# Performance work log

Measured on AMD Instinct MI355X. Metric: run time of the kernel, lower is better.

The kernel has to match this reference:

```python
import jax, jax.numpy as jnp
import numpy as np

A, S, D, V = 128, 512, 768, 30522
NL, LW = 10, 5  # n label categories, words per category
MASK_ID = 103
NEG = -1e30


def setup_inputs() -> dict:
    key = jax.random.key(0)
    ks = jax.random.split(key, 12)
    scale = 0.02
    input_ids = jax.random.randint(ks[0], (A, S), 0, 30000)
    input_ids = jnp.where(input_ids == MASK_ID, MASK_ID + 1, input_ids)  # strip accidental masks
    mask_pos = jax.random.randint(ks[1], (A,), 1, 3)  # one [MASK] per row, before position 3
    input_ids = input_ids.at[jnp.arange(A), mask_pos].set(MASK_ID)
    length = jax.random.randint(ks[2], (A,), 1, 400)
    bert_out = jax.random.normal(ks[3], (A, S, D), jnp.float32)
    label_words = jax.random.randint(ks[4], (NL, LW), 0, V)
    return {
        "bert_out": bert_out,
        "input_ids": input_ids,
        "length": length,
        "label_words": label_words,
        "W_senti": jax.random.normal(ks[5], (2, D), jnp.float32) * scale,
        "b_senti": jnp.zeros((2,), jnp.float32),
        "W_dense": jax.random.normal(ks[6], (D, 2 * D), jnp.float32) * scale,
        "b_dense": jnp.zeros((D,), jnp.float32),
        "W_prob": jax.random.normal(ks[7], (V, D), jnp.float32) * scale,
        "b_prob": jnp.zeros((V,), jnp.float32),
        "W_lab": jax.random.normal(ks[8], (NL, 2, LW), jnp.float32) * scale,
    }


def reference(bert_out, input_ids, length, label_words,
              W_senti, b_senti, W_dense, b_dense, W_prob, b_prob, W_lab):
    a, s, d = bert_out.shape
    # pooler = [CLS] hidden state -> senti head (dropout is identity in eval)
    senti_out = bert_out[:, 0] @ W_senti.T + b_senti  # [A,2]

    # gather the (single) [MASK] token hidden state per sample
    mask_pos = jnp.argmax(input_ids == MASK_ID, axis=1)        # [A]
    mask_logit = bert_out[jnp.arange(a), mask_pos]             # [A,D]

    # ragged attention pool over bert_out[i, 3:3+length[i]] vectorized via masking
    pos = jnp.arange(s)
    valid = (pos[None, :] >= 3) & (pos[None, :] < 3 + length[:, None])  # [A,S]
    scores = jnp.einsum('asd,ad->as', bert_out, mask_logit)
    scores = jnp.where(valid, scores, NEG)
    w = jax.nn.softmax(scores, axis=1)                         # [A,S]
    att = jnp.einsum('as,asd->ad', w, bert_out)                # [A,D]

    x = jnp.concatenate([att, mask_logit], axis=-1)            # [A,2D]
    h = jnp.tanh(x @ W_dense.T + b_dense)                      # [A,D]
    p = jnp.tanh(h @ W_prob.T + b_prob)                        # [A,V]

    # per-category label-word gather + small no-bias linear, stacked on dim 2
    lp = p[:, label_words]                                     # [A,NL,LW]
    out = jnp.einsum('alw,lkw->akl', lp, W_lab)                # [A,2,NL]
    return senti_out, out
```

## Files before the change

kernel.cpp:

```cpp
#include <hip/hip_runtime.h>
#include <stdint.h>

#define A_ 128
#define S_ 512
#define D_ 768
#define MASKID 103

typedef short bf16x8_t __attribute__((ext_vector_type(8)));
typedef float floatx4_t __attribute__((ext_vector_type(4)));

__device__ __forceinline__ unsigned short f2bf(float f) {
    union { unsigned int u; float f; } v; v.f = f;
    unsigned int u = v.u;
    return (unsigned short)((u + 0x7fffu + ((u >> 16) & 1u)) >> 16);
}

__global__ __launch_bounds__(256) void attn_part(
    const float* __restrict__ bert,
    const int* __restrict__ ids,
    const int* __restrict__ length,
    const int* __restrict__ label_words,
    const float* __restrict__ W_prob,
    const float* __restrict__ b_prob,
    unsigned short* __restrict__ ws_Wpw,
    float* __restrict__ ws_bp,
    int* __restrict__ ws_mask_pos,
    float* __restrict__ part_m,
    float* __restrict__ part_l,
    float* __restrict__ part_acc)
{
    int bx = blockIdx.x;
    int tid = threadIdx.x;
    if (bx >= A_ * 8) {
        int r = bx - A_ * 8;
        if (r < 50) {
            int word = label_words[r];
            const float* src = W_prob + (size_t)word * D_;
            for (int j = tid; j < D_; j += 256) ws_Wpw[r * D_ + j] = f2bf(src[j]);
            if (tid == 0) ws_bp[r] = b_prob[word];
        } else {
            for (int j = tid; j < D_; j += 256) ws_Wpw[r * D_ + j] = 0;
            if (tid == 0) ws_bp[r] = 0.f;
        }
        return;
    }
    int a = bx >> 3, c = bx & 7;
    int wave = tid >> 6, lane = tid & 63;
    int d0 = lane * 4;

    __shared__ int s_minpos;
    __shared__ float red_m[4], red_l[4];
    __shared__ float red_acc[4][D_];

    if (tid == 0) s_minpos = S_;
    __syncthreads();
    for (int p = tid; p < S_; p += 256)
        if (ids[a * S_ + p] == MASKID) atomicMin(&s_minpos, p);
    __syncthreads();
    int mp = (s_minpos >= S_) ? 0 : s_minpos;

    const float* base = bert + (size_t)a * S_ * D_;

    float ml[12];
    {
        const float* q = base + (size_t)mp * D_ + d0;
        float4 v0 = *(const float4*)(q);
        float4 v1 = *(const float4*)(q + 256);
        float4 v2 = *(const float4*)(q + 512);
        ml[0]=v0.x; ml[1]=v0.y; ml[2]=v0.z; ml[3]=v0.w;
        ml[4]=v1.x; ml[5]=v1.y; ml[6]=v1.z; ml[7]=v1.w;
        ml[8]=v2.x; ml[9]=v2.y; ml[10]=v2.z; ml[11]=v2.w;
    }
    int len = length[a]; if (len > S_ - 3) len = S_ - 3;

    float m = -3.0e38f, l = 0.f;
    float acc[12];
#pragma unroll
    for (int k = 0; k < 12; k++) acc[k] = 0.f;

    int v = c + 8 * wave;
    for (; v + 32 < len; v += 64) {
        const float* qa = base + (size_t)(3 + v) * D_ + d0;
        const float* qb = base + (size_t)(3 + v + 32) * D_ + d0;
        float4 a0 = *(const float4*)(qa);
        float4 a1 = *(const float4*)(qa + 256);
        float4 a2 = *(const float4*)(qa + 512);
        float4 b0 = *(const float4*)(qb);
        float4 b1 = *(const float4*)(qb + 256);
        float4 b2 = *(const float4*)(qb + 512);
        float ra[12], rb[12];
        ra[0]=a0.x; ra[1]=a0.y; ra[2]=a0.z; ra[3]=a0.w;
        ra[4]=a1.x; ra[5]=a1.y; ra[6]=a1.z; ra[7]=a1.w;
        ra[8]=a2.x; ra[9]=a2.y; ra[10]=a2.z; ra[11]=a2.w;
        rb[0]=b0.x; rb[1]=b0.y; rb[2]=b0.z; rb[3]=b0.w;
        rb[4]=b1.x; rb[5]=b1.y; rb[6]=b1.z; rb[7]=b1.w;
        rb[8]=b2.x; rb[9]=b2.y; rb[10]=b2.z; rb[11]=b2.w;
        float pa = 0.f, pb = 0.f;
#pragma unroll
        for (int k = 0; k < 12; k++) { pa = fmaf(ra[k], ml[k], pa); pb = fmaf(rb[k], ml[k], pb); }
#pragma unroll
        for (int off = 32; off >= 1; off >>= 1) {
            pa += __shfl_xor(pa, off, 64);
            pb += __shfl_xor(pb, off, 64);
        }
        float mn = fmaxf(m, fmaxf(pa, pb));
        float alpha = __expf(m - mn);
        float wa = __expf(pa - mn);
        float wb = __expf(pb - mn);
        l = l * alpha + wa + wb;
#pragma unroll
        for (int k = 0; k < 12; k++)
            acc[k] = fmaf(acc[k], alpha, fmaf(wa, ra[k], wb * rb[k]));
        m = mn;
    }
    for (; v < len; v += 32) {
        const float* qa = base + (size_t)(3 + v) * D_ + d0;
        float4 a0 = *(const float4*)(qa);
        float4 a1 = *(const float4*)(qa + 256);
        float4 a2 = *(const float4*)(qa + 512);
        float ra[12];
        ra[0]=a0.x; ra[1]=a0.y; ra[2]=a0.z; ra[3]=a0.w;
        ra[4]=a1.x; ra[5]=a1.y; ra[6]=a1.z; ra[7]=a1.w;
        ra[8]=a2.x; ra[9]=a2.y; ra[10]=a2.z; ra[11]=a2.w;
        float pa = 0.f;
#pragma unroll
        for (int k = 0; k < 12; k++) pa = fmaf(ra[k], ml[k], pa);
#pragma unroll
        for (int off = 32; off >= 1; off >>= 1)
            pa += __shfl_xor(pa, off, 64);
        float mn = fmaxf(m, pa);
        float alpha = __expf(m - mn);
        float wa = __expf(pa - mn);
        l = l * alpha + wa;
#pragma unroll
        for (int k = 0; k < 12; k++) acc[k] = fmaf(acc[k], alpha, wa * ra[k]);
        m = mn;
    }
    if (lane == 0) { red_m[wave] = m; red_l[wave] = l; }
#pragma unroll
    for (int j = 0; j < 3; j++) {
        floatx4_t t = { acc[4*j], acc[4*j+1], acc[4*j+2], acc[4*j+3] };
        *(floatx4_t*)&red_acc[wave][d0 + 256 * j] = t;
    }
    __syncthreads();

    float m0 = red_m[0], m1 = red_m[1], m2 = red_m[2], m3 = red_m[3];
    float M = fmaxf(fmaxf(m0, m1), fmaxf(m2, m3));
    float f0 = __expf(m0 - M), f1 = __expf(m1 - M);
    float f2 = __expf(m2 - M), f3 = __expf(m3 - M);
    int pc = (a * 8 + c) * D_;
#pragma unroll
    for (int e = 0; e < 3; e++) {
        int d = tid + 256 * e;
        part_acc[pc + d] = f0 * red_acc[0][d] + f1 * red_acc[1][d]
                         + f2 * red_acc[2][d] + f3 * red_acc[3][d];
    }
    if (tid == 0) {
        part_m[a * 8 + c] = M;
        part_l[a * 8 + c] = f0 * red_l[0] + f1 * red_l[1] + f2 * red_l[2] + f3 * red_l[3];
        if (c == 0) ws_mask_pos[a] = mp;
    }
}

__global__ __launch_bounds__(256) void merge_kernel(
    const float* __restrict__ bert,
    const float* __restrict__ W_senti,
    const float* __restrict__ b_senti,
    const int* __restrict__ ws_mask_pos,
    const float* __restrict__ part_m,
    const float* __restrict__ part_l,
    const float* __restrict__ part_acc,
    unsigned short* __restrict__ ws_x,
    float* __restrict__ d_out)
{
    int a = blockIdx.x, tid = threadIdx.x;
    float mc[8], lc[8];
#pragma unroll
    for (int c = 0; c < 8; c++) { mc[c] = part_m[a * 8 + c]; lc[c] = part_l[a * 8 + c]; }
    float M = mc[0];
#pragma unroll
    for (int c = 1; c < 8; c++) M = fmaxf(M, mc[c]);
    float fac[8]; float denom = 0.f;
#pragma unroll
    for (int c = 0; c < 8; c++) { fac[c] = __expf(mc[c] - M); denom += fac[c] * lc[c]; }
    float inv = 1.0f / fmaxf(denom, 1e-30f);

    const float* pa = part_acc + (size_t)a * 8 * D_;
    int mp = ws_mask_pos[a];
    const float* mrow = bert + ((size_t)a * S_ + mp) * D_;
#pragma unroll
    for (int e = 0; e < 3; e++) {
        int d = tid + 256 * e;
        float s = 0.f;
#pragma unroll
        for (int c = 0; c < 8; c++) s += fac[c] * pa[c * D_ + d];
        ws_x[a * 1536 + d] = f2bf(s * inv);
        ws_x[a * 1536 + D_ + d] = f2bf(mrow[d]);
    }
    const float* r0 = bert + (size_t)a * S_ * D_;
    float p0 = 0.f, p1 = 0.f;
#pragma unroll
    for (int e = 0; e < 3; e++) {
        int d = tid + 256 * e;
        float b = r0[d];
        p0 = fmaf(b, W_senti[d], p0);
        p1 = fmaf(b, W_senti[D_ + d], p1);
    }
#pragma unroll
    for (int off = 32; off >= 1; off >>= 1) {
        p0 += __shfl_xor(p0, off, 64);
        p1 += __shfl_xor(p1, off, 64);
    }
    __shared__ float s0[4], s1[4];
    int wave = tid >> 6, lane = tid & 63;
    if (lane == 0) { s0[wave] = p0; s1[wave] = p1; }
    __syncthreads();
    if (tid == 0) {
        d_out[a * 2 + 0] = s0[0] + s0[1] + s0[2] + s0[3] + b_senti[0];
        d_out[a * 2 + 1] = s1[0] + s1[1] + s1[2] + s1[3] + b_senti[1];
    }
}

__global__ __launch_bounds__(256) void dense_kernel(
    const unsigned short* __restrict__ ws_x,
    const float* __restrict__ W_dense,
    const float* __restrict__ b_dense,
    unsigned short* __restrict__ ws_h)
{
    int tid = threadIdx.x;
    int wave = tid >> 6, lane = tid & 63;
    int r = lane & 15, q = lane >> 4;
    int tile_local = wave >> 1, kh = wave & 1;
    int T = blockIdx.x * 2 + tile_local;
    int m_t = T / 48, n_t = T % 48;
    const bf16x8_t* Ap = (const bf16x8_t*)(ws_x + (size_t)(m_t * 16 + r) * 1536 + kh * 768 + q * 8);
    const float* Bp = W_dense + (size_t)(n_t * 16 + r) * 1536 + kh * 768 + q * 8;
    floatx4_t acc = {0.f, 0.f, 0.f, 0.f};
#pragma unroll
    for (int kk = 0; kk < 24; kk++) {
        bf16x8_t av = Ap[kk * 4];
        float4 b0 = *(const float4*)(Bp + kk * 32);
        float4 b1 = *(const float4*)(Bp + kk * 32 + 4);
        bf16x8_t bv;
        bv[0] = (short)f2bf(b0.x); bv[1] = (short)f2bf(b0.y);
        bv[2] = (short)f2bf(b0.z); bv[3] = (short)f2bf(b0.w);
        bv[4] = (short)f2bf(b1.x); bv[5] = (short)f2bf(b1.y);
        bv[6] = (short)f2bf(b1.z); bv[7] = (short)f2bf(b1.w);
        acc = __builtin_amdgcn_mfma_f32_16x16x32_bf16(av, bv, acc, 0, 0, 0);
    }
    __shared__ float part[4][256];
#pragma unroll
    for (int reg = 0; reg < 4; reg++)
        part[wave][(q * 4 + reg) * 16 + r] = acc[reg];
    __syncthreads();
    for (int t = tid; t < 512; t += 256) {
        int tl = t >> 8, id2 = t & 255;
        float sum = part[tl * 2][id2] + part[tl * 2 + 1][id2];
        int T2 = blockIdx.x * 2 + tl;
        int mt2 = T2 / 48, nt2 = T2 % 48;
        int row = id2 >> 4, col = id2 & 15;
        int n = nt2 * 16 + col;
        float h = tanhf(sum + b_dense[n]);
        ws_h[(size_t)(mt2 * 16 + row) * 768 + n] = f2bf(h);
    }
}

__global__ __launch_bounds__(256) void label_kernel(
    const unsigned short* __restrict__ ws_h,
    const unsigned short* __restrict__ ws_Wpw,
    const float* __restrict__ ws_bp,
    const float* __restrict__ W_lab,
    float* __restrict__ d_out)
{
    int tid = threadIdx.x;
    int wave = tid >> 6, lane = tid & 63;
    int r = lane & 15, q = lane >> 4;
    int m_t = blockIdx.x;
    int n_t = wave;
    const bf16x8_t* Ap = (const bf16x8_t*)(ws_h + (size_t)(m_t * 16 + r) * 768 + q * 8);
    const bf16x8_t* Bp = (const bf16x8_t*)(ws_Wpw + (size_t)(n_t * 16 + r) * 768 + q * 8);
    floatx4_t acc = {0.f, 0.f, 0.f, 0.f};
#pragma unroll
    for (int kk = 0; kk < 24; kk++)
        acc = __builtin_amdgcn_mfma_f32_16x16x32_bf16(Ap[kk * 4], Bp[kk * 4], acc, 0, 0, 0);
    __shared__ float lp_s[16][64];
    int col = n_t * 16 + r;
    float bp = ws_bp[col];
#pragma unroll
    for (int reg = 0; reg < 4; reg++)
        lp_s[q * 4 + reg][col] = tanhf(acc[reg] + bp);
    __syncthreads();
    for (int t = tid; t < 320; t += 256) {
        int al = t / 20, rem = t % 20;
        int k = rem / 10, lb = rem % 10;
        float s = 0.f;
#pragma unroll
        for (int w = 0; w < 5; w++)
            s = fmaf(lp_s[al][lb * 5 + w], W_lab[(lb * 2 + k) * 5 + w], s);
        d_out[256 + (m_t * 16 + al) * 20 + rem] = s;
    }
}

extern "C" void kernel_launch(void* const* d_in, const int* in_sizes, int n_in,
                              void* d_out, int out_size, void* d_ws, size_t ws_size,
                              hipStream_t stream) {
    const float* bert    = (const float*)d_in[0];
    const int* ids       = (const int*)d_in[1];
    const int* length    = (const int*)d_in[2];
    const int* label_words = (const int*)d_in[3];
    const float* W_senti = (const float*)d_in[4];
    const float* b_senti = (const float*)d_in[5];
    const float* W_dense = (const float*)d_in[6];
    const float* b_dense = (const float*)d_in[7];
    const float* W_prob  = (const float*)d_in[8];
    const float* b_prob  = (const float*)d_in[9];
    const float* W_lab   = (const float*)d_in[10];
    float* out = (float*)d_out;

    char* ws = (char*)d_ws;
    unsigned short* ws_x   = (unsigned short*)(ws + 0);
    unsigned short* ws_h   = (unsigned short*)(ws + 393216);
    unsigned short* ws_Wpw = (unsigned short*)(ws + 589824);
    float*          ws_bp  = (float*)(ws + 688128);
    int*     ws_mask_pos   = (int*)(ws + 688384);
    float*          part_m = (float*)(ws + 688896);
    float*          part_l = (float*)(ws + 692992);
    float*        part_acc = (float*)(ws + 697088);

    attn_part<<<A_ * 8 + 64, 256, 0, stream>>>(bert, ids, length, label_words,
        W_prob, b_prob, ws_Wpw, ws_bp, ws_mask_pos, part_m, part_l, part_acc);
    merge_kernel<<<A_, 256, 0, stream>>>(bert, W_senti, b_senti, ws_mask_pos,
        part_m, part_l, part_acc, ws_x, out);
    dense_kernel<<<192, 256, 0, stream>>>(ws_x, W_dense, b_dense, ws_h);
    label_kernel<<<8, 256, 0, stream>>>(ws_h, ws_Wpw, ws_bp, W_lab, out);
}
```

Before: 324.8 us.

## Split attention into 16 chunks, pre-convert W_dense to bf16, move senti head

Raises the per-sample split of the attention pool from 8 to 16 blocks for more parallelism. W_dense is converted to bf16 by the spare blocks of the first kernel, so the dense GEMM reads bf16 directly and splits K across four waves per tile. The senti head and the mask-row copy move into the attention kernel, which shrinks the merge kernel. The cost is more partial results to merge and extra workspace for the converted weight.

```diff
diff --git a/kernel.cpp b/kernel.cpp
--- a/kernel.cpp
+++ b/kernel.cpp
@@ -4,6 +4,7 @@
 #define A_ 128
 #define S_ 512
 #define D_ 768
+#define C_ 16
 #define MASKID 103
 
 typedef short bf16x8_t __attribute__((ext_vector_type(8)));
@@ -22,17 +23,22 @@
     const int* __restrict__ label_words,
     const float* __restrict__ W_prob,
     const float* __restrict__ b_prob,
+    const float* __restrict__ W_dense,
+    const float* __restrict__ W_senti,
+    const float* __restrict__ b_senti,
     unsigned short* __restrict__ ws_Wpw,
     float* __restrict__ ws_bp,
-    int* __restrict__ ws_mask_pos,
+    unsigned short* __restrict__ ws_Wd,
+    unsigned short* __restrict__ ws_x,
     float* __restrict__ part_m,
     float* __restrict__ part_l,
-    float* __restrict__ part_acc)
+    float* __restrict__ part_acc,
+    float* __restrict__ d_out)
 {
     int bx = blockIdx.x;
     int tid = threadIdx.x;
-    if (bx >= A_ * 8) {
-        int r = bx - A_ * 8;
+    if (bx >= A_ * C_) {
+        int r = bx - A_ * C_;
         if (r < 50) {
             int word = label_words[r];
             const float* src = W_prob + (size_t)word * D_;
@@ -42,9 +48,18 @@
             for (int j = tid; j < D_; j += 256) ws_Wpw[r * D_ + j] = 0;
             if (tid == 0) ws_bp[r] = 0.f;
         }
+        const float4* src4 = (const float4*)(W_dense + (size_t)r * 18432);
+        ushort4* dst4 = (ushort4*)(ws_Wd + (size_t)r * 18432);
+#pragma unroll
+        for (int it = 0; it < 18; it++) {
+            float4 v = src4[tid + 256 * it];
+            ushort4 o;
+            o.x = f2bf(v.x); o.y = f2bf(v.y); o.z = f2bf(v.z); o.w = f2bf(v.w);
+            dst4[tid + 256 * it] = o;
+        }
         return;
     }
-    int a = bx >> 3, c = bx & 7;
+    int a = bx >> 4, c = bx & 15;
     int wave = tid >> 6, lane = tid & 63;
     int d0 = lane * 4;
 
@@ -52,14 +67,49 @@
     __shared__ float red_m[4], red_l[4];
     __shared__ float red_acc[4][D_];
 
+    const float* base = bert + (size_t)a * S_ * D_;
+
+    if (c == 1 && wave == 0) {
+        const float* q = base + d0;
+        float4 v0 = *(const float4*)(q);
+        float4 v1 = *(const float4*)(q + 256);
+        float4 v2 = *(const float4*)(q + 512);
+        float4 u0 = *(const float4*)(W_senti + d0);
+        float4 u1 = *(const float4*)(W_senti + d0 + 256);
+        float4 u2 = *(const float4*)(W_senti + d0 + 512);
+        float4 t0 = *(const float4*)(W_senti + D_ + d0);
+        float4 t1 = *(const float4*)(W_senti + D_ + d0 + 256);
+        float4 t2 = *(const float4*)(W_senti + D_ + d0 + 512);
+        float rv[12], w0[12], w1[12];
+        rv[0]=v0.x; rv[1]=v0.y; rv[2]=v0.z; rv[3]=v0.w;
+        rv[4]=v1.x; rv[5]=v1.y; rv[6]=v1.z; rv[7]=v1.w;
+        rv[8]=v2.x; rv[9]=v2.y; rv[10]=v2.z; rv[11]=v2.w;
+        w0[0]=u0.x; w0[1]=u0.y; w0[2]=u0.z; w0[3]=u0.w;
+        w0[4]=u1.x; w0[5]=u1.y; w0[6]=u1.z; w0[7]=u1.w;
+        w0[8]=u2.x; w0[9]=u2.y; w0[10]=u2.z; w0[11]=u2.w;
+        w1[0]=t0.x; w1[1]=t0.y; w1[2]=t0.z; w1[3]=t0.w;
+        w1[4]=t1.x; w1[5]=t1.y; w1[6]=t1.z; w1[7]=t1.w;
+        w1[8]=t2.x; w1[9]=t2.y; w1[10]=t2.z; w1[11]=t2.w;
+        float p0 = 0.f, p1 = 0.f;
+#pragma unroll
+        for (int k = 0; k < 12; k++) { p0 = fmaf(rv[k], w0[k], p0); p1 = fmaf(rv[k], w1[k], p1); }
+#pragma unroll
+        for (int off = 32; off >= 1; off >>= 1) {
+            p0 += __shfl_xor(p0, off, 64);
+            p1 += __shfl_xor(p1, off, 64);
+        }
+        if (lane == 0) {
+            d_out[a * 2 + 0] = p0 + b_senti[0];
+            d_out[a * 2 + 1] = p1 + b_senti[1];
+        }
+    }
+
     if (tid == 0) s_minpos = S_;
     __syncthreads();
     for (int p = tid; p < S_; p += 256)
         if (ids[a * S_ + p] == MASKID) atomicMin(&s_minpos, p);
     __syncthreads();
     int mp = (s_minpos >= S_) ? 0 : s_minpos;
-
-    const float* base = bert + (size_t)a * S_ * D_;
 
     float ml[12];
     {
@@ -71,6 +121,15 @@
         ml[4]=v1.x; ml[5]=v1.y; ml[6]=v1.z; ml[7]=v1.w;
         ml[8]=v2.x; ml[9]=v2.y; ml[10]=v2.z; ml[11]=v2.w;
     }
+    if (c == 0 && wave == 0) {
+#pragma unroll
+        for (int j = 0; j < 3; j++) {
+            ushort4 o;
+            o.x = f2bf(ml[4*j]);   o.y = f2bf(ml[4*j+1]);
+            o.z = f2bf(ml[4*j+2]); o.w = f2bf(ml[4*j+3]);
+            *(ushort4*)(ws_x + (size_t)a * 1536 + D_ + d0 + 256 * j) = o;
+        }
+    }
     int len = length[a]; if (len > S_ - 3) len = S_ - 3;
 
     float m = -3.0e38f, l = 0.f;
@@ -78,10 +137,10 @@
 #pragma unroll
     for (int k = 0; k < 12; k++) acc[k] = 0.f;
 
-    int v = c + 8 * wave;
-    for (; v + 32 < len; v += 64) {
+    int v = c + 16 * wave;
+    for (; v + 64 < len; v += 128) {
         const float* qa = base + (size_t)(3 + v) * D_ + d0;
-        const float* qb = base + (size_t)(3 + v + 32) * D_ + d0;
+        const float* qb = base + (size_t)(3 + v + 64) * D_ + d0;
         float4 a0 = *(const float4*)(qa);
         float4 a1 = *(const float4*)(qa + 256);
         float4 a2 = *(const float4*)(qa + 512);
@@ -113,7 +172,7 @@
             acc[k] = fmaf(acc[k], alpha, fmaf(wa, ra[k], wb * rb[k]));
         m = mn;
     }
-    for (; v < len; v += 32) {
+    for (; v < len; v += 64) {
         const float* qa = base + (size_t)(3 + v) * D_ + d0;
         float4 a0 = *(const float4*)(qa);
         float4 a1 = *(const float4*)(qa + 256);
@@ -148,7 +207,7 @@
     float M = fmaxf(fmaxf(m0, m1), fmaxf(m2, m3));
     float f0 = __expf(m0 - M), f1 = __expf(m1 - M);
     float f2 = __expf(m2 - M), f3 = __expf(m3 - M);
-    int pc = (a * 8 + c) * D_;
+    int pc = (a * C_ + c) * D_;
 #pragma unroll
     for (int e = 0; e < 3; e++) {
         int d = tid + 256 * e;
@@ -156,113 +215,67 @@
                          + f2 * red_acc[2][d] + f3 * red_acc[3][d];
     }
     if (tid == 0) {
-        part_m[a * 8 + c] = M;
-        part_l[a * 8 + c] = f0 * red_l[0] + f1 * red_l[1] + f2 * red_l[2] + f3 * red_l[3];
-        if (c == 0) ws_mask_pos[a] = mp;
+        part_m[a * C_ + c] = M;
+        part_l[a * C_ + c] = f0 * red_l[0] + f1 * red_l[1] + f2 * red_l[2] + f3 * red_l[3];
     }
 }
 
 __global__ __launch_bounds__(256) void merge_kernel(
-    const float* __restrict__ bert,
-    const float* __restrict__ W_senti,
-    const float* __restrict__ b_senti,
-    const int* __restrict__ ws_mask_pos,
     const float* __restrict__ part_m,
     const float* __restrict__ part_l,
     const float* __restrict__ part_acc,
-    unsigned short* __restrict__ ws_x,
-    float* __restrict__ d_out)
+    unsigned short* __restrict__ ws_x)
 {
     int a = blockIdx.x, tid = threadIdx.x;
-    float mc[8], lc[8];
-#pragma unroll
-    for (int c = 0; c < 8; c++) { mc[c] = part_m[a * 8 + c]; lc[c] = part_l[a * 8 + c]; }
+    float mc[C_], lc[C_];
+#pragma unroll
+    for (int c = 0; c < C_; c++) { mc[c] = part_m[a * C_ + c]; lc[c] = part_l[a * C_ + c]; }
     float M = mc[0];
 #pragma unroll
-    for (int c = 1; c < 8; c++) M = fmaxf(M, mc[c]);
-    float fac[8]; float denom = 0.f;
-#pragma unroll
-    for (int c = 0; c < 8; c++) { fac[c] = __expf(mc[c] - M); denom += fac[c] * lc[c]; }
+    for (int c = 1; c < C_; c++) M = fmaxf(M, mc[c]);
+    float fac[C_]; float denom = 0.f;
+#pragma unroll
+    for (int c = 0; c < C_; c++) { fac[c] = __expf(mc[c] - M); denom += fac[c] * lc[c]; }
     float inv = 1.0f / fmaxf(denom, 1e-30f);
 
-    const float* pa = part_acc + (size_t)a * 8 * D_;
-    int mp = ws_mask_pos[a];
-    const float* mrow = bert + ((size_t)a * S_ + mp) * D_;
+    const float* pa = part_acc + (size_t)a * C_ * D_;
 #pragma unroll
     for (int e = 0; e < 3; e++) {
         int d = tid + 256 * e;
         float s = 0.f;
 #pragma unroll
-        for (int c = 0; c < 8; c++) s += fac[c] * pa[c * D_ + d];
-        ws_x[a * 1536 + d] = f2bf(s * inv);
-        ws_x[a * 1536 + D_ + d] = f2bf(mrow[d]);
-    }
-    const float* r0 = bert + (size_t)a * S_ * D_;
-    float p0 = 0.f, p1 = 0.f;
-#pragma unroll
-    for (int e = 0; e < 3; e++) {
-        int d = tid + 256 * e;
-        float b = r0[d];
-        p0 = fmaf(b, W_senti[d], p0);
-        p1 = fmaf(b, W_senti[D_ + d], p1);
-    }
-#pragma unroll
-    for (int off = 32; off >= 1; off >>= 1) {
-        p0 += __shfl_xor(p0, off, 64);
-        p1 += __shfl_xor(p1, off, 64);
-    }
-    __shared__ float s0[4], s1[4];
-    int wave = tid >> 6, lane = tid & 63;
-    if (lane == 0) { s0[wave] = p0; s1[wave] = p1; }
-    __syncthreads();
-    if (tid == 0) {
-        d_out[a * 2 + 0] = s0[0] + s0[1] + s0[2] + s0[3] + b_senti[0];
-        d_out[a * 2 + 1] = s1[0] + s1[1] + s1[2] + s1[3] + b_senti[1];
+        for (int c = 0; c < C_; c++) s = fmaf(fac[c], pa[c * D_ + d], s);
+        ws_x[(size_t)a * 1536 + d] = f2bf(s * inv);
     }
 }
 
 __global__ __launch_bounds__(256) void dense_kernel(
     const unsigned short* __restrict__ ws_x,
-    const float* __restrict__ W_dense,
+    const unsigned short* __restrict__ ws_Wd,
     const float* __restrict__ b_dense,
     unsigned short* __restrict__ ws_h)
 {
     int tid = threadIdx.x;
     int wave = tid >> 6, lane = tid & 63;
     int r = lane & 15, q = lane >> 4;
-    int tile_local = wave >> 1, kh = wave & 1;
-    int T = blockIdx.x * 2 + tile_local;
+    int T = blockIdx.x;
     int m_t = T / 48, n_t = T % 48;
-    const bf16x8_t* Ap = (const bf16x8_t*)(ws_x + (size_t)(m_t * 16 + r) * 1536 + kh * 768 + q * 8);
-    const float* Bp = W_dense + (size_t)(n_t * 16 + r) * 1536 + kh * 768 + q * 8;
+    const bf16x8_t* Ap = (const bf16x8_t*)(ws_x  + (size_t)(m_t * 16 + r) * 1536 + wave * 384 + q * 8);
+    const bf16x8_t* Bp = (const bf16x8_t*)(ws_Wd + (size_t)(n_t * 16 + r) * 1536 + wave * 384 + q * 8);
     floatx4_t acc = {0.f, 0.f, 0.f, 0.f};
 #pragma unroll
-    for (int kk = 0; kk < 24; kk++) {
-        bf16x8_t av = Ap[kk * 4];
-        float4 b0 = *(const float4*)(Bp + kk * 32);
-        float4 b1 = *(const float4*)(Bp + kk * 32 + 4);
-        bf16x8_t bv;
-        bv[0] = (short)f2bf(b0.x); bv[1] = (short)f2bf(b0.y);
-        bv[2] = (short)f2bf(b0.z); bv[3] = (short)f2bf(b0.w);
-        bv[4] = (short)f2bf(b1.x); bv[5] = (short)f2bf(b1.y);
-        bv[6] = (short)f2bf(b1.z); bv[7] = (short)f2bf(b1.w);
-        acc = __builtin_amdgcn_mfma_f32_16x16x32_bf16(av, bv, acc, 0, 0, 0);
-    }
+    for (int kk = 0; kk < 12; kk++)
+        acc = __builtin_amdgcn_mfma_f32_16x16x32_bf16(Ap[kk * 4], Bp[kk * 4], acc, 0, 0, 0);
     __shared__ float part[4][256];
 #pragma unroll
     for (int reg = 0; reg < 4; reg++)
         part[wave][(q * 4 + reg) * 16 + r] = acc[reg];
     __syncthreads();
-    for (int t = tid; t < 512; t += 256) {
-        int tl = t >> 8, id2 = t & 255;
-        float sum = part[tl * 2][id2] + part[tl * 2 + 1][id2];
-        int T2 = blockIdx.x * 2 + tl;
-        int mt2 = T2 / 48, nt2 = T2 % 48;
-        int row = id2 >> 4, col = id2 & 15;
-        int n = nt2 * 16 + col;
-        float h = tanhf(sum + b_dense[n]);
-        ws_h[(size_t)(mt2 * 16 + row) * 768 + n] = f2bf(h);
-    }
+    float sum = part[0][tid] + part[1][tid] + part[2][tid] + part[3][tid];
+    int row = tid >> 4, col = tid & 15;
+    int n = n_t * 16 + col;
+    float h = tanhf(sum + b_dense[n]);
+    ws_h[(size_t)(m_t * 16 + row) * D_ + n] = f2bf(h);
 }
 
 __global__ __launch_bounds__(256) void label_kernel(
@@ -322,15 +335,15 @@
     unsigned short* ws_h   = (unsigned short*)(ws + 393216);
     unsigned short* ws_Wpw = (unsigned short*)(ws + 589824);
     float*          ws_bp  = (float*)(ws + 688128);
-    int*     ws_mask_pos   = (int*)(ws + 688384);
-    float*          part_m = (float*)(ws + 688896);
-    float*          part_l = (float*)(ws + 692992);
-    float*        part_acc = (float*)(ws + 697088);
-
-    attn_part<<<A_ * 8 + 64, 256, 0, stream>>>(bert, ids, length, label_words,
-        W_prob, b_prob, ws_Wpw, ws_bp, ws_mask_pos, part_m, part_l, part_acc);
-    merge_kernel<<<A_, 256, 0, stream>>>(bert, W_senti, b_senti, ws_mask_pos,
-        part_m, part_l, part_acc, ws_x, out);
-    dense_kernel<<<192, 256, 0, stream>>>(ws_x, W_dense, b_dense, ws_h);
+    unsigned short* ws_Wd  = (unsigned short*)(ws + 688384);
+    float*          part_m = (float*)(ws + 3047680);
+    float*          part_l = (float*)(ws + 3055872);
+    float*        part_acc = (float*)(ws + 3064064);
+
+    attn_part<<<A_ * C_ + 64, 256, 0, stream>>>(bert, ids, length, label_words,
+        W_prob, b_prob, W_dense, W_senti, b_senti,
+        ws_Wpw, ws_bp, ws_Wd, ws_x, part_m, part_l, part_acc, out);
+    merge_kernel<<<A_, 256, 0, stream>>>(part_m, part_l, part_acc, ws_x);
+    dense_kernel<<<384, 256, 0, stream>>>(ws_x, ws_Wd, b_dense, ws_h);
     label_kernel<<<8, 256, 0, stream>>>(ws_h, ws_Wpw, ws_bp, W_lab, out);
 }
```

After: 323.7 us (median of 2 runs). About the same (-0.3%).
